# Performance work log

Hardware: AMD Instinct MI355X
Metric: run time of the kernel (lower is better)

The kernel has to match this reference:

```python
import jax, jax.numpy as jnp
import numpy as np

NUM_NODES = 100000
NUM_EDGES = 400000
EPS = 1e-9


def _find(parent, u):
    # chase parent pointers to the root (no path compression; parent is
    # immutable within one find, so this terminates because union-by-rank
    # keeps the forest acyclic)
    return jax.lax.while_loop(lambda v: parent[v] != v, lambda v: parent[v], u)


def _kruskal(scores, edge_index, num_nodes):
    """Greedy Kruskal over edges sorted by descending score, via union-find.
    Returns b in {0,1}^E with exactly (num_nodes-1) ones if the graph is
    connected (fewer otherwise), identical acceptance set to the torch loop."""
    E = scores.shape[0]
    order = jnp.argsort(-scores)  # descending
    src = edge_index[0].astype(jnp.int32)
    dst = edge_index[1].astype(jnp.int32)
    max_used = jnp.int32(num_nodes - 1)

    def step(carry, idx):
        parent, rank, b, used = carry
        i = src[idx]
        j = dst[idx]
        ru = _find(parent, i)
        rv = _find(parent, j)
        accept = (ru != rv) & (used < max_used)
        ri = rank[ru]
        rj = rank[rv]
        # union by rank: if ri<rj attach ru under rv, else attach rv under ru;
        # if ranks equal, root ru gains rank (matches the torch union())
        child = jnp.where(ri < rj, ru, rv)
        root = jnp.where(ri < rj, rv, ru)
        parent = parent.at[child].set(jnp.where(accept, root, parent[child]))
        rank = rank.at[root].add(jnp.where(accept & (ri == rj), jnp.int32(1), jnp.int32(0)))
        b = b.at[idx].set(accept.astype(b.dtype))
        used = used + accept.astype(used.dtype)
        return (parent, rank, b, used), None

    parent0 = jnp.arange(num_nodes, dtype=jnp.int32)
    rank0 = jnp.zeros(num_nodes, dtype=jnp.int32)
    b0 = jnp.zeros(E, dtype=scores.dtype)
    (parent, rank, b, used), _ = jax.lax.scan(step, (parent0, rank0, b0, jnp.int32(0)), order)
    return b


def setup_inputs() -> dict:
    key = jax.random.key(0)
    k1, k2, k3 = jax.random.split(key, 3)
    s = jax.random.normal(k1, (NUM_EDGES,), dtype=jnp.float32)
    u = jax.random.uniform(k2, (NUM_EDGES,), dtype=jnp.float32)
    edge_index = jax.random.randint(k3, (2, NUM_EDGES), 0, NUM_NODES, dtype=jnp.int32)
    return {"s": s, "u": u, "edge_index": edge_index, "num_nodes": NUM_NODES}


def reference(s, u, edge_index, num_nodes):
    s_prob = jax.nn.sigmoid(s)
    gumbel = -jnp.log(-jnp.log(u + EPS) + EPS)
    scores = s_prob + gumbel
    return _kruskal(scores, edge_index, num_nodes)
```

## Files before the change

kernel.cpp:

```cpp
#include <hip/hip_runtime.h>
#include <stdint.h>

#define V_NODES 100000
#define MAX_ROUNDS 13
#define TB 256
#define RPT 4
#define TBL 2048
#define TBL_FROM 3

struct alignas(16) Rec { unsigned long long k; unsigned int a, b; };

__device__ __forceinline__ unsigned long long make_key(float sv, float uv, int id) {
    float sp = 1.0f / (1.0f + expf(-sv));
    float g  = -logf(-logf(uv + 1e-9f) + 1e-9f);
    unsigned int b = __float_as_uint(sp + g);
    unsigned int m = (b & 0x80000000u) ? ~b : (b | 0x80000000u);
    return ((unsigned long long)(~m) << 19) | (unsigned long long)(unsigned)id;
}

__device__ __forceinline__ int find_root(const int* __restrict__ parent, int v) {
    int p = parent[v];
    int pp = parent[p];
    while (p != pp) { p = pp; pp = parent[p]; }
    return p;
}

__device__ __forceinline__ void gbid(unsigned long long* __restrict__ best,
                                     unsigned int* __restrict__ guess,
                                     unsigned int root, unsigned long long k) {
    unsigned int kh = (unsigned int)(k >> 32);
    unsigned int g = guess[root];
    if (kh > g) return;
    if (kh < g) guess[root] = kh;
    atomicMin(&best[root], k);
}

__global__ void k_scan0(const float* __restrict__ s, const float* __restrict__ u,
                        const int* __restrict__ src, const int* __restrict__ dst,
                        float* __restrict__ out, unsigned long long* __restrict__ best,
                        unsigned int* __restrict__ guess,
                        Rec* __restrict__ recs, int* __restrict__ parent,
                        int* __restrict__ flags, int E) {
    int base = (blockIdx.x * TB + threadIdx.x) * RPT;

    float sv[RPT], uv[RPT];
    unsigned int a[RPT], b[RPT];
    #pragma unroll
    for (int j = 0; j < RPT; ++j) {
        int e = base + j;
        if (e < E) { sv[j] = s[e]; uv[j] = u[e]; a[j] = src[e]; b[j] = dst[e]; }
    }

    Rec r[RPT];
    #pragma unroll
    for (int j = 0; j < RPT; ++j) {
        int e = base + j;
        if (e >= E) continue;
        r[j].k = make_key(sv[j], uv[j], e);
        r[j].a = a[j]; r[j].b = b[j];
        recs[e] = r[j];
        out[e] = 0.0f;
        if (e < V_NODES) parent[e] = e;
        if (e < MAX_ROUNDS) flags[e] = (e == 0) ? 1 : 0;
    }

    #pragma unroll
    for (int j = 0; j < RPT; ++j) {
        int e = base + j;
        if (e >= E || a[j] == b[j]) continue;
        gbid(best, guess, a[j], r[j].k);
        gbid(best, guess, b[j], r[j].k);
    }
}

__global__ void k_scan(const int* __restrict__ parent,
                       unsigned long long* __restrict__ bestC,
                       unsigned int* __restrict__ guess,
                       Rec* __restrict__ recs, int* __restrict__ flags,
                       int r, int E) {
    __shared__ int sflag;
    __shared__ unsigned int tag[TBL];
    __shared__ unsigned long long tkey[TBL];
    if (flags[r - 1] == 0) return;
    const bool useTbl = (r >= TBL_FROM);
    if (useTbl)
        for (int t = threadIdx.x; t < TBL; t += TB) { tag[t] = 0xFFFFFFFFu; tkey[t] = ~0ULL; }
    if (threadIdx.x == 0) sflag = 0;
    __syncthreads();

    int base = (blockIdx.x * TB + threadIdx.x) * RPT;
    bool cross = false;

    Rec rec[RPT];
    int pa[RPT], pb[RPT];
    bool live[RPT];
    #pragma unroll
    for (int j = 0; j < RPT; ++j) {
        int i = base + j;
        if (i < E) rec[j] = recs[i];
        else { rec[j].a = 0; rec[j].b = 0; }
        live[j] = (rec[j].a != rec[j].b);
    }
    #pragma unroll
    for (int j = 0; j < RPT; ++j)
        if (live[j]) { pa[j] = parent[rec[j].a]; pb[j] = parent[rec[j].b]; }

    auto bid = [&](unsigned int root, unsigned long long k) {
        if (useTbl) {
            unsigned int s1 = root & (TBL - 1);
            unsigned int prev = atomicCAS(&tag[s1], 0xFFFFFFFFu, root);
            if (prev == 0xFFFFFFFFu || prev == root) {
                atomicMin(&tkey[s1], k);
                return;
            }
            unsigned int s2 = (root * 2654435761u >> 19) & (TBL - 1);
            prev = atomicCAS(&tag[s2], 0xFFFFFFFFu, root);
            if (prev == 0xFFFFFFFFu || prev == root) {
                atomicMin(&tkey[s2], k);
                return;
            }
        }
        gbid(bestC, guess, root, k);
    };

    #pragma unroll
    for (int j = 0; j < RPT; ++j) {
        if (!live[j]) continue;
        int i = base + j;
        int ra = pa[j], rb = pb[j];
        int p = parent[ra]; while (ra != p) { ra = p; p = parent[ra]; }
        p = parent[rb];     while (rb != p) { rb = p; p = parent[rb]; }
        if (ra == rb) {
            *(uint2*)&recs[i].a = make_uint2((unsigned)ra, (unsigned)ra);
        } else {
            cross = true;
            if ((unsigned)ra != rec[j].a || (unsigned)rb != rec[j].b)
                *(uint2*)&recs[i].a = make_uint2((unsigned)ra, (unsigned)rb);
            bid((unsigned)ra, rec[j].k);
            bid((unsigned)rb, rec[j].k);
        }
    }
    if (cross) sflag = 1;
    __syncthreads();

    if (useTbl)
        for (int t = threadIdx.x; t < TBL; t += TB) {
            unsigned int rt = tag[t];
            if (rt != 0xFFFFFFFFu) gbid(bestC, guess, rt, tkey[t]);
        }
    if (threadIdx.x == 0 && sflag) flags[r] = 1;
}

__global__ void k_choose(const int* __restrict__ src, const int* __restrict__ dst,
                         int* __restrict__ parent,
                         const unsigned long long* __restrict__ bestC,
                         float* __restrict__ out, const int* __restrict__ flags,
                         int r) {
    if (flags[r] == 0) return;
    int v = blockIdx.x * blockDim.x + threadIdx.x;
    if (v >= V_NODES) return;
    unsigned long long k = bestC[v];
    if ((unsigned)(k >> 51) != 0u) return;
    int id = (int)(unsigned int)(k & 0x7FFFFu);
    int a0 = src[id], b0 = dst[id];
    int ru = find_root(parent, a0);
    int rv = find_root(parent, b0);
    if (ru != a0) parent[a0] = ru;
    if (rv != b0) parent[b0] = rv;
    int other = (ru == v) ? rv : ru;
    out[id] = 1.0f;
    if (bestC[other] != k || v > other) {
        if (other != v) parent[v] = other;
    }
}

extern "C" void kernel_launch(void* const* d_in, const int* in_sizes, int n_in,
                              void* d_out, int out_size, void* d_ws, size_t ws_size,
                              hipStream_t stream) {
    const float* s  = (const float*)d_in[0];
    const float* u  = (const float*)d_in[1];
    const int*   ei = (const int*)d_in[2];
    const int E = in_sizes[0];
    const int* src = ei;
    const int* dst = ei + E;
    float* out = (float*)d_out;

    char* ws = (char*)d_ws;
    Rec* recs = (Rec*)ws;
    unsigned long long* bestAll = (unsigned long long*)(recs + E);
    int* parent = (int*)(bestAll + (size_t)MAX_ROUNDS * V_NODES);
    unsigned int* guessAll = (unsigned int*)(parent + V_NODES);
    int* flags  = (int*)(guessAll + (size_t)MAX_ROUNDS * V_NODES);

    const int gE4 = (E + TB * RPT - 1) / (TB * RPT);
    const int gV  = (V_NODES + TB - 1) / TB;

    k_scan0<<<gE4, TB, 0, stream>>>(s, u, src, dst, out, bestAll, guessAll,
                                    recs, parent, flags, E);
    k_choose<<<gV, TB, 0, stream>>>(src, dst, parent, bestAll, out, flags, 0);

    for (int r = 1; r < MAX_ROUNDS; ++r) {
        unsigned long long* best_r = bestAll + (size_t)r * V_NODES;
        unsigned int* guess_r = guessAll + (size_t)r * V_NODES;
        k_scan<<<gE4, TB, 0, stream>>>(parent, best_r, guess_r,
                                       recs, flags, r, E);
        k_choose<<<gV, TB, 0, stream>>>(src, dst, parent, best_r, out, flags, r);
    }
}
```

Before: 272.7 us.

## Compact surviving roots into a worklist for later choose rounds

```diff
diff --git a/kernel.cpp b/kernel.cpp
--- a/kernel.cpp
+++ b/kernel.cpp
@@ -62,6 +62,7 @@
         out[e] = 0.0f;
         if (e < V_NODES) parent[e] = e;
         if (e < MAX_ROUNDS) flags[e] = (e == 0) ? 1 : 0;
+        else if (e >= 16 && e < 32) flags[e] = 0;
     }
 
     #pragma unroll
@@ -151,16 +152,13 @@
     if (threadIdx.x == 0 && sflag) flags[r] = 1;
 }
 
-__global__ void k_choose(const int* __restrict__ src, const int* __restrict__ dst,
-                         int* __restrict__ parent,
-                         const unsigned long long* __restrict__ bestC,
-                         float* __restrict__ out, const int* __restrict__ flags,
-                         int r) {
-    if (flags[r] == 0) return;
-    int v = blockIdx.x * blockDim.x + threadIdx.x;
-    if (v >= V_NODES) return;
+__device__ __forceinline__ bool choose_body(int v, const int* __restrict__ src,
+                                            const int* __restrict__ dst,
+                                            int* __restrict__ parent,
+                                            const unsigned long long* __restrict__ bestC,
+                                            float* __restrict__ out) {
     unsigned long long k = bestC[v];
-    if ((unsigned)(k >> 51) != 0u) return;
+    if ((unsigned)(k >> 51) != 0u) return false;
     int id = (int)(unsigned int)(k & 0x7FFFFu);
     int a0 = src[id], b0 = dst[id];
     int ru = find_root(parent, a0);
@@ -169,9 +167,60 @@
     if (rv != b0) parent[b0] = rv;
     int other = (ru == v) ? rv : ru;
     out[id] = 1.0f;
-    if (bestC[other] != k || v > other) {
-        if (other != v) parent[v] = other;
-    }
+    bool hook = (bestC[other] != k || v > other) && (other != v);
+    if (hook) parent[v] = other;
+    return !hook;
+}
+
+__device__ __forceinline__ void block_append(bool win, int v,
+                                             int* __restrict__ listOut,
+                                             int* __restrict__ cntOut) {
+    __shared__ int wbase[TB / 64];
+    __shared__ int sbase;
+    unsigned long long mask = __ballot(win);
+    int lane = threadIdx.x & 63;
+    int wid  = threadIdx.x >> 6;
+    if (lane == 0) wbase[wid] = (int)__popcll(mask);
+    __syncthreads();
+    if (threadIdx.x == 0) {
+        int acc = 0;
+        #pragma unroll
+        for (int w = 0; w < TB / 64; ++w) { int c = wbase[w]; wbase[w] = acc; acc += c; }
+        sbase = acc ? atomicAdd(cntOut, acc) : 0;
+    }
+    __syncthreads();
+    if (win) {
+        int pos = sbase + wbase[wid] + (int)__popcll(mask & ((1ull << lane) - 1ull));
+        listOut[pos] = v;
+    }
+}
+
+__global__ void k_choose0(const int* __restrict__ src, const int* __restrict__ dst,
+                          int* __restrict__ parent,
+                          const unsigned long long* __restrict__ bestC,
+                          float* __restrict__ out,
+                          int* __restrict__ listOut, int* __restrict__ cntOut) {
+    int v = blockIdx.x * TB + threadIdx.x;
+    bool win = false;
+    if (v < V_NODES) win = choose_body(v, src, dst, parent, bestC, out);
+    block_append(win, v, listOut, cntOut);
+}
+
+__global__ void k_chooseL(const int* __restrict__ src, const int* __restrict__ dst,
+                          int* __restrict__ parent,
+                          const unsigned long long* __restrict__ bestC,
+                          float* __restrict__ out,
+                          const int* __restrict__ listIn, const int* __restrict__ cntIn,
+                          int* __restrict__ listOut, int* __restrict__ cntOut) {
+    int n = *cntIn;
+    if (n == 0) return;
+    int idx = blockIdx.x * TB + threadIdx.x;
+    bool win = false; int v = 0;
+    if (idx < n) {
+        v = listIn[idx];
+        win = choose_body(v, src, dst, parent, bestC, out);
+    }
+    block_append(win, v, listOut, cntOut);
 }
 
 extern "C" void kernel_launch(void* const* d_in, const int* in_sizes, int n_in,
@@ -191,19 +240,27 @@
     int* parent = (int*)(bestAll + (size_t)MAX_ROUNDS * V_NODES);
     unsigned int* guessAll = (unsigned int*)(parent + V_NODES);
     int* flags  = (int*)(guessAll + (size_t)MAX_ROUNDS * V_NODES);
+    int* listA  = flags + 32;
+    int* listB  = listA + V_NODES;
 
     const int gE4 = (E + TB * RPT - 1) / (TB * RPT);
     const int gV  = (V_NODES + TB - 1) / TB;
 
+    int* cnt = flags + 16;
+
     k_scan0<<<gE4, TB, 0, stream>>>(s, u, src, dst, out, bestAll, guessAll,
                                     recs, parent, flags, E);
-    k_choose<<<gV, TB, 0, stream>>>(src, dst, parent, bestAll, out, flags, 0);
+    k_choose0<<<gV, TB, 0, stream>>>(src, dst, parent, bestAll, out,
+                                     listA, cnt + 0);
 
     for (int r = 1; r < MAX_ROUNDS; ++r) {
         unsigned long long* best_r = bestAll + (size_t)r * V_NODES;
         unsigned int* guess_r = guessAll + (size_t)r * V_NODES;
+        const int* lin  = (r & 1) ? listA : listB;
+        int* lout       = (r & 1) ? listB : listA;
         k_scan<<<gE4, TB, 0, stream>>>(parent, best_r, guess_r,
                                        recs, flags, r, E);
-        k_choose<<<gV, TB, 0, stream>>>(src, dst, parent, best_r, out, flags, r);
-    }
-}
+        k_chooseL<<<gV, TB, 0, stream>>>(src, dst, parent, best_r, out,
+                                         lin, cnt + (r - 1), lout, cnt + r);
+    }
+}
```

Result: slower. 287.0 us (+5.2%).
